# Kernel optimization log

Measured on AMD Instinct MI355X. Metric: run time of the kernel, lower is better.

## Reference

```python
import jax, jax.numpy as jnp
import numpy as np

D_MODEL = 2048
N_HEADS = 16
D_HEAD = D_MODEL // N_HEADS
FF = 4 * D_MODEL
B, L = 2, 2048


def setup_inputs() -> dict:
    key = jax.random.key(0)
    ks = jax.random.split(key, 12)
    s = 0.02
    inp = {
        "x": jax.random.normal(ks[0], (B, L, D_MODEL), jnp.float32),
        "rope_cos": jnp.cos(jnp.arange(L)[:, None] / (10000.0 ** (jnp.arange(D_HEAD) / D_HEAD))).astype(jnp.float32),
        "rope_sin": jnp.sin(jnp.arange(L)[:, None] / (10000.0 ** (jnp.arange(D_HEAD) / D_HEAD))).astype(jnp.float32),
        "mask": jnp.ones((B, L), jnp.int32),
        "w_norm1": jnp.ones((D_MODEL,), jnp.float32),
        "w_norm2": jnp.ones((D_MODEL,), jnp.float32),
        # linear weights stored as [in, out] (transposed torch layout)
        "wq": jax.random.normal(ks[1], (D_MODEL, D_MODEL), jnp.float32) * s,
        "wk": jax.random.normal(ks[2], (D_MODEL, D_MODEL), jnp.float32) * s,
        "wv": jax.random.normal(ks[3], (D_MODEL, D_MODEL), jnp.float32) * s,
        "wo": jax.random.normal(ks[4], (D_MODEL, D_MODEL), jnp.float32) * s,
        "w_ff1": jax.random.normal(ks[5], (D_MODEL, FF), jnp.float32) * s,
        "w_ff2": jax.random.normal(ks[6], (FF, D_MODEL), jnp.float32) * s,
    }
    return inp


def _rmsnorm(x, w):
    eps = jnp.finfo(x.dtype).eps
    return x * jax.lax.rsqrt(jnp.mean(x * x, axis=-1, keepdims=True) + eps) * w


def _rotate_half(x):
    x1, x2 = jnp.split(x, 2, axis=-1)
    return jnp.concatenate([-x2, x1], axis=-1)


def reference(x, rope_cos, rope_sin, mask, w_norm1, w_norm2, wq, wk, wv, wo, w_ff1, w_ff2):
    b, l, d = x.shape
    h, dh = N_HEADS, D_HEAD

    residual = x
    xn = _rmsnorm(x, w_norm1)
    # project and split heads: [B, H, L, DH]
    q = (xn @ wq).reshape(b, l, h, dh).transpose(0, 2, 1, 3)
    k = (xn @ wk).reshape(b, l, h, dh).transpose(0, 2, 1, 3)
    v = (xn @ wv).reshape(b, l, h, dh).transpose(0, 2, 1, 3)

    cos = rope_cos[None, None]  # [1,1,L,DH]
    sin = rope_sin[None, None]
    q = q * cos + _rotate_half(q) * sin
    k = k * cos + _rotate_half(k) * sin

    scores = jnp.einsum("bhqd,bhkd->bhqk", q, k) * (dh ** -0.5)
    causal = jnp.tril(jnp.ones((l, l), bool))  # allowed positions
    allowed = causal[None, None] & (mask[:, None, None, :] != 0)
    scores = jnp.where(allowed, scores, -jnp.inf)
    attn = jax.nn.softmax(scores, axis=-1)  # dropout is identity in eval

    out = jnp.einsum("bhqk,bhkd->bhqd", attn, v)
    out = out.transpose(0, 2, 1, 3).reshape(b, l, d)
    x = residual + out @ wo

    xn2 = _rmsnorm(x, w_norm2)
    ff = jax.nn.silu(xn2 @ w_ff1) @ w_ff2
    return x + ff
```

## Files before the change

kernel.cpp:

```cpp
#include <hip/hip_runtime.h>


typedef __bf16 bf16;
typedef __bf16 bf16x8 __attribute__((ext_vector_type(8)));
typedef float  f32x4  __attribute__((ext_vector_type(4)));

__device__ __forceinline__ void gload16(const void* g, void* l) {
  __builtin_amdgcn_global_load_lds((const __attribute__((address_space(1))) void*)g,
                                   (__attribute__((address_space(3))) void*)l,
                                   16, 0, 0);
}

#define CBAR asm volatile("" ::: "memory")
#define WAITV(N) asm volatile("s_waitcnt vmcnt(" #N ")" ::: "memory")
#define LGKM0 asm volatile("s_waitcnt lgkmcnt(0)" ::: "memory")
#define BARR { CBAR; __builtin_amdgcn_s_barrier(); CBAR; }

__global__ __launch_bounds__(256) void rmsnorm_to_bf16(
    const float* __restrict__ x, const float* __restrict__ w, bf16* __restrict__ out)
{
  const int D = 2048;
  const int row = blockIdx.x;
  const int tid = threadIdx.x;
  const float* xr = x + (size_t)row * D;
  float4 a = ((const float4*)xr)[tid * 2];
  float4 c = ((const float4*)xr)[tid * 2 + 1];
  float ss = a.x*a.x + a.y*a.y + a.z*a.z + a.w*a.w
           + c.x*c.x + c.y*c.y + c.z*c.z + c.w*c.w;
  #pragma unroll
  for (int m = 1; m < 64; m <<= 1) ss += __shfl_xor(ss, m, 64);
  __shared__ float red[4];
  if ((tid & 63) == 0) red[tid >> 6] = ss;
  __syncthreads();
  float tot = red[0] + red[1] + red[2] + red[3];
  float rms = rsqrtf(tot * (1.0f / D) + 1.1920929e-7f);
  const float* wr = w + tid * 8;
  float vals[8] = {a.x, a.y, a.z, a.w, c.x, c.y, c.z, c.w};
  bf16x8 o;
  #pragma unroll
  for (int j = 0; j < 8; ++j) o[j] = (bf16)(vals[j] * rms * wr[j]);
  *(bf16x8*)(out + (size_t)row * D + tid * 8) = o;
}

__global__ __launch_bounds__(256) void transpose_to_bf16(
    const float* __restrict__ in, bf16* __restrict__ out, int R, int C)
{
  __shared__ float tile[32][33];
  const int tx = threadIdx.x, ty = threadIdx.y;
  const int c0 = blockIdx.x * 32, r0 = blockIdx.y * 32;
  #pragma unroll
  for (int i = 0; i < 4; ++i)
    tile[ty + i * 8][tx] = in[(size_t)(r0 + ty + i * 8) * C + c0 + tx];
  __syncthreads();
  #pragma unroll
  for (int i = 0; i < 4; ++i)
    out[(size_t)(c0 + ty + i * 8) * R + r0 + tx] = (bf16)tile[tx][ty + i * 8];
}

__global__ __launch_bounds__(256) void v_transpose(
    const bf16* __restrict__ v, bf16* __restrict__ vt)
{
  const int L = 2048, DM = 2048;
  __shared__ bf16 tile[32][33];
  const int tx = threadIdx.x, ty = threadIdx.y;
  const int k0 = blockIdx.x * 32;
  const int d0 = blockIdx.y * 32;
  const int bh = blockIdx.z;
  const int b = bh >> 4, h = bh & 15;
  #pragma unroll
  for (int i = 0; i < 4; ++i)
    tile[ty + i * 8][tx] = v[(size_t)(b * L + k0 + ty + i * 8) * DM + h * 128 + d0 + tx];
  __syncthreads();
  #pragma unroll
  for (int i = 0; i < 4; ++i) {
    const int d = d0 + ty + i * 8;
    const int key = k0 + tx;
    const int keysw = (key & ~63) | (((((key >> 3) & 7) ^ (d & 7)) << 3)) | (key & 7);
    vt[(size_t)(bh * 128 + d) * L + keysw] = tile[tx][ty + i * 8];
  }
}

template<int EPI>
__global__ __launch_bounds__(512, 1) void gemm256(
    const bf16* __restrict__ A, const bf16* __restrict__ Bt,
    void* Cout, const float* __restrict__ resid, int M, int N, int K)
{
  __shared__ bf16 sA[2][2][128 * 64];
  __shared__ bf16 sB[2][2][128 * 64];

  const int tid = threadIdx.x, lane = tid & 63, w = tid >> 6;
  const int wm = w >> 2, wn = w & 3;
  const int lo = lane & 15, hi = lane >> 4;
  const int lo7 = lo & 7;

  const int nbn = N >> 8;
  const int nwg = gridDim.x;
  int swz = blockIdx.x;
  if ((nwg & 7) == 0) { const int cpx = nwg >> 3; swz = (swz & 7) * cpx + (swz >> 3); }
  const int bm = swz / nbn, bn = swz % nbn;

  const int r0 = tid >> 3,         s0 = (tid & 7) ^ (r0 & 7);
  const int r1 = (512 + tid) >> 3, s1 = ((512 + tid) & 7) ^ (r1 & 7);
  const bf16* Ab = A  + (size_t)(bm * 256) * K;
  const bf16* Bb = Bt + (size_t)(bn * 256) * K;
  const size_t o0 = (size_t)r0 * K + s0 * 8;
  const size_t o1 = (size_t)r1 * K + s1 * 8;
  const int dst0 = (w * 64) * 8, dst1 = (512 + w * 64) * 8;
  const size_t rhK = (size_t)128 * K;

  bf16x8 a0[2][4], a1[2][4], b0[2][2], b1[2][2];
  f32x4 acc[8][4] = {};
  const int NT = K >> 6;

  auto stageA = [&](int b, int rh, int kt) {
    const bf16* s = Ab + rh * rhK + (size_t)kt * 64;
    gload16(s + o0, &sA[b][rh][dst0]);
    gload16(s + o1, &sA[b][rh][dst1]);
  };
  auto stageB = [&](int b, int rh, int kt) {
    const bf16* s = Bb + rh * rhK + (size_t)kt * 64;
    gload16(s + o0, &sB[b][rh][dst0]);
    gload16(s + o1, &sB[b][rh][dst1]);
  };
  auto loadA = [&](bf16x8 (&d)[2][4], int b, int rh) {
    #pragma unroll
    for (int ks = 0; ks < 2; ++ks)
      #pragma unroll
      for (int m = 0; m < 4; ++m) {
        const int row = wm * 64 + m * 16 + lo;
        d[ks][m] = *(const bf16x8*)&sA[b][rh][row * 64 + (((ks * 4 + hi) ^ lo7) << 3)];
      }
  };
  auto loadB = [&](bf16x8 (&d)[2][2], int b, int rh) {
    #pragma unroll
    for (int ks = 0; ks < 2; ++ks)
      #pragma unroll
      for (int nj = 0; nj < 2; ++nj) {
        const int row = wn * 32 + nj * 16 + lo;
        d[ks][nj] = *(const bf16x8*)&sB[b][rh][row * 64 + (((ks * 4 + hi) ^ lo7) << 3)];
      }
  };
  auto mfma16 = [&](bf16x8 (&a)[2][4], bf16x8 (&bf)[2][2], int mb, int nb2) {
    __builtin_amdgcn_s_setprio(1);
    #pragma unroll
    for (int ks = 0; ks < 2; ++ks)
      #pragma unroll
      for (int m = 0; m < 4; ++m)
        #pragma unroll
        for (int nj = 0; nj < 2; ++nj)
          acc[mb + m][nb2 + nj] = __builtin_amdgcn_mfma_f32_16x16x32_bf16(
              a[ks][m], bf[ks][nj], acc[mb + m][nb2 + nj], 0, 0, 0);
    __builtin_amdgcn_s_setprio(0);
  };

  stageA(0, 0, 0); stageB(0, 0, 0); stageB(0, 1, 0); stageA(0, 1, 0);
  WAITV(0);
  BARR;
  loadA(a0, 0, 0);
  loadB(b0, 0, 0);

  for (int t = 0; t < NT; ++t) {
    const int buf = t & 1, nb = buf ^ 1;
    const bool st = (t + 1 < NT);
    loadB(b1, buf, 1);
    if (st) stageA(nb, 0, t + 1);
    mfma16(a0, b0, 0, 0);
    if (st) { WAITV(2); } else { WAITV(0); }
    BARR;
    loadA(a1, buf, 1);
    if (st) stageB(nb, 0, t + 1);
    mfma16(a0, b1, 0, 2);
    BARR;
    if (st) stageB(nb, 1, t + 1);
    mfma16(a1, b1, 4, 2);
    if (st) { WAITV(2); }
    BARR;
    mfma16(a1, b0, 4, 0);
    if (st) {
      loadA(a0, nb, 0);
      loadB(b0, nb, 0);
      stageA(nb, 1, t + 1);
      WAITV(2);
    }
    BARR;
  }

  #pragma unroll
  for (int mi = 0; mi < 8; ++mi) {
    #pragma unroll
    for (int j = 0; j < 4; ++j) {
      const size_t row = (size_t)(bm * 256 + (mi >> 2) * 128 + wm * 64 + (mi & 3) * 16 + hi * 4 + j);
      #pragma unroll
      for (int ni = 0; ni < 4; ++ni) {
        const int col = bn * 256 + (ni >> 1) * 128 + wn * 32 + (ni & 1) * 16 + lo;
        const float v = acc[mi][ni][j];
        if constexpr (EPI == 2) {
          ((bf16*)Cout)[row * (size_t)N + col] = (bf16)(v / (1.0f + __expf(-v)));
        } else {
          ((bf16*)Cout)[(size_t)(col >> 11) * 8388608 + row * 2048 + (col & 2047)] = (bf16)v;
        }
      }
    }
  }
}

__global__ __launch_bounds__(512, 1) void gemm128(
    const bf16* __restrict__ A, const bf16* __restrict__ Bt,
    float* __restrict__ Cout, const float* __restrict__ resid, int M, int N, int K)
{
  __shared__ bf16 sA[2][128 * 64];
  __shared__ bf16 sB[2][2][128 * 64];

  const int tid = threadIdx.x, lane = tid & 63, w = tid >> 6;
  const int wm = w >> 2, wn = w & 3;
  const int lo = lane & 15, hi = lane >> 4;
  const int lo7 = lo & 7;

  const int nbn = N >> 8;
  const int nwg = gridDim.x;
  int swz = blockIdx.x;
  if ((nwg & 7) == 0) { const int cpx = nwg >> 3; swz = (swz & 7) * cpx + (swz >> 3); }
  const int bm = swz / nbn, bn = swz % nbn;

  const int r0 = tid >> 3,         s0 = (tid & 7) ^ (r0 & 7);
  const int r1 = (512 + tid) >> 3, s1 = ((512 + tid) & 7) ^ (r1 & 7);
  const bf16* Ab = A  + (size_t)(bm * 128) * K;
  const bf16* Bb = Bt + (size_t)(bn * 256) * K;
  const size_t o0 = (size_t)r0 * K + s0 * 8;
  const size_t o1 = (size_t)r1 * K + s1 * 8;
  const int dst0 = (w * 64) * 8, dst1 = (512 + w * 64) * 8;
  const size_t nhK = (size_t)128 * K;

  bf16x8 afA[2][4], b0[2][2], b1[2][2];
  f32x4 acc[4][4] = {};
  const int NT = K >> 6;

  auto stageA = [&](int b, int kt) {
    const bf16* s = Ab + (size_t)kt * 64;
    gload16(s + o0, &sA[b][dst0]);
    gload16(s + o1, &sA[b][dst1]);
  };
  auto stageB = [&](int b, int nh, int kt) {
    const bf16* s = Bb + nh * nhK + (size_t)kt * 64;
    gload16(s + o0, &sB[b][nh][dst0]);
    gload16(s + o1, &sB[b][nh][dst1]);
  };
  auto loadA = [&](int b) {
    #pragma unroll
    for (int ks = 0; ks < 2; ++ks)
      #pragma unroll
      for (int m = 0; m < 4; ++m) {
        const int row = wm * 64 + m * 16 + lo;
        afA[ks][m] = *(const bf16x8*)&sA[b][row * 64 + (((ks * 4 + hi) ^ lo7) << 3)];
      }
  };
  auto loadB = [&](bf16x8 (&d)[2][2], int b, int nh) {
    #pragma unroll
    for (int ks = 0; ks < 2; ++ks)
      #pragma unroll
      for (int nj = 0; nj < 2; ++nj) {
        const int row = wn * 32 + nj * 16 + lo;
        d[ks][nj] = *(const bf16x8*)&sB[b][nh][row * 64 + (((ks * 4 + hi) ^ lo7) << 3)];
      }
  };
  auto mfma16 = [&](bf16x8 (&bf)[2][2], int nb2) {
    __builtin_amdgcn_s_setprio(1);
    #pragma unroll
    for (int ks = 0; ks < 2; ++ks)
      #pragma unroll
      for (int m = 0; m < 4; ++m)
        #pragma unroll
        for (int nj = 0; nj < 2; ++nj)
          acc[m][nb2 + nj] = __builtin_amdgcn_mfma_f32_16x16x32_bf16(
              afA[ks][m], bf[ks][nj], acc[m][nb2 + nj], 0, 0, 0);
    __builtin_amdgcn_s_setprio(0);
  };

  stageA(0, 0); stageB(0, 0, 0); stageB(0, 1, 0);
  WAITV(0);
  BARR;

  for (int t = 0; t < NT; ++t) {
    const int buf = t & 1, nb = buf ^ 1;
    const bool st = (t + 1 < NT);
    loadA(buf);
    loadB(b0, buf, 0);
    if (st) stageA(nb, t + 1);
    BARR; LGKM0;
    mfma16(b0, 0);
    if (st) { WAITV(2); } else { WAITV(0); }
    BARR;
    loadB(b1, buf, 1);
    if (st) { stageB(nb, 0, t + 1); stageB(nb, 1, t + 1); }
    BARR; LGKM0;
    mfma16(b1, 2);
    if (st) { WAITV(2); }
    BARR;
  }

  #pragma unroll
  for (int mi = 0; mi < 4; ++mi) {
    #pragma unroll
    for (int j = 0; j < 4; ++j) {
      const size_t row = (size_t)(bm * 128 + wm * 64 + mi * 16 + hi * 4 + j);
      const size_t ro = row * (size_t)N;
      #pragma unroll
      for (int ni = 0; ni < 4; ++ni) {
        const int col = bn * 256 + (ni >> 1) * 128 + wn * 32 + (ni & 1) * 16 + lo;
        Cout[ro + col] = acc[mi][ni][j] + resid[ro + col];
      }
    }
  }
}

__global__ __launch_bounds__(256) void rope_qk(
    bf16* q, const bf16* __restrict__ k, bf16* __restrict__ kswz,
    const float* __restrict__ cs, const float* __restrict__ sn)
{
  const int L = 2048, DM = 2048;
  const int idx = blockIdx.x * 256 + threadIdx.x;
  const int m = idx >> 7;
  const int rem = idx & 127;
  const int h = rem >> 3, t8 = rem & 7;
  const int pos = m & (L - 1);
  const int d0 = t8 * 8;
  const float* cb = cs + (size_t)pos * 128 + d0;
  const float* sb = sn + (size_t)pos * 128 + d0;
  float4 c1a = *(const float4*)(cb);      float4 c1b = *(const float4*)(cb + 4);
  float4 c2a = *(const float4*)(cb + 64); float4 c2b = *(const float4*)(cb + 68);
  float4 s1a = *(const float4*)(sb);      float4 s1b = *(const float4*)(sb + 4);
  float4 s2a = *(const float4*)(sb + 64); float4 s2b = *(const float4*)(sb + 68);
  float c1[8] = {c1a.x,c1a.y,c1a.z,c1a.w,c1b.x,c1b.y,c1b.z,c1b.w};
  float c2[8] = {c2a.x,c2a.y,c2a.z,c2a.w,c2b.x,c2b.y,c2b.z,c2b.w};
  float s1[8] = {s1a.x,s1a.y,s1a.z,s1a.w,s1b.x,s1b.y,s1b.z,s1b.w};
  float s2[8] = {s2a.x,s2a.y,s2a.z,s2a.w,s2b.x,s2b.y,s2b.z,s2b.w};
  const size_t base = (size_t)m * DM + h * 128 + d0;

  {
    bf16x8 x1 = *(bf16x8*)(q + base);
    bf16x8 x2 = *(bf16x8*)(q + base + 64);
    bf16x8 o1, o2;
    #pragma unroll
    for (int j = 0; j < 8; ++j) {
      const float a = (float)x1[j], b = (float)x2[j];
      o1[j] = (bf16)(a * c1[j] - b * s1[j]);
      o2[j] = (bf16)(b * c2[j] + a * s2[j]);
    }
    *(bf16x8*)(q + base) = o1;
    *(bf16x8*)(q + base + 64) = o2;
  }
  {
    bf16x8 x1 = *(const bf16x8*)(k + base);
    bf16x8 x2 = *(const bf16x8*)(k + base + 64);
    bf16x8 o1, o2;
    #pragma unroll
    for (int j = 0; j < 8; ++j) {
      const float a = (float)x1[j], b = (float)x2[j];
      o1[j] = (bf16)(a * c1[j] - b * s1[j]);
      o2[j] = (bf16)(b * c2[j] + a * s2[j]);
    }
    const int s = pos & 15;
    const int p1 = t8 ^ s;
    const int p2 = (8 + t8) ^ s;
    bf16* kr = kswz + (size_t)m * DM + h * 128;
    *(bf16x8*)(kr + p1 * 8) = o1;
    *(bf16x8*)(kr + p2 * 8) = o2;
  }
}

__global__ __launch_bounds__(256, 2) void attn_fwd(
    const bf16* __restrict__ Q, const bf16* __restrict__ Kswz,
    const bf16* __restrict__ VT, const int* __restrict__ mask,
    bf16* __restrict__ O)
{
  const int L = 2048, DM = 2048;
  __shared__ bf16 Kt[2][64 * 128];
  __shared__ bf16 Vt[2][128 * 64];
  __shared__ bf16 Plds[4][16 * 64];

  const int tid = threadIdx.x, lane = tid & 63, w = tid >> 6;
  const int lo = lane & 15, hi = lane >> 4;
  const int s7 = lo & 7;
  const int n = blockIdx.x;
  const int xcd = n & 7, slot = n >> 3;
  const int bh = xcd + 8 * (slot >> 5);
  const int tile = 31 - (slot & 31);
  const int b = bh >> 4, h = bh & 15;
  const int qrow = tile * 64 + w * 16;
  const float scale = 0.08838834764831845f;
  const float NEG_INF = -__builtin_inff();

  bf16x8 qf[4];
  {
    const bf16* qb = Q + (size_t)(b * L + qrow + lo) * DM + h * 128;
    #pragma unroll
    for (int ds = 0; ds < 4; ++ds) qf[ds] = *(const bf16x8*)(qb + ds * 32 + hi * 8);
  }

  float mrow[4] = {NEG_INF, NEG_INF, NEG_INF, NEG_INF};
  float lrow[4] = {0.f, 0.f, 0.f, 0.f};
  f32x4 oacc[8] = {};

  const bf16* vsrc[4];
  const bf16* ksrc[4];
  #pragma unroll
  for (int i = 0; i < 4; ++i) {
    const int gv = i * 256 + tid;
    vsrc[i] = VT + (size_t)(bh * 128 + (gv >> 3)) * L + (gv & 7) * 8;
    const int gk = i * 256 + tid;
    ksrc[i] = Kswz + (size_t)(b * L + (gk >> 4)) * DM + h * 128 + (gk & 15) * 8;
  }

  #pragma unroll
  for (int i = 0; i < 4; ++i) {
    gload16(ksrc[i], &Kt[0][(i * 256 + w * 64) * 8]);
    gload16(vsrc[i], &Vt[0][(i * 256 + w * 64) * 8]);
  }
  __syncthreads();

  const int nkt = tile + 1;
  for (int kt = 0; kt < nkt; ++kt) {
    const int buf = kt & 1;
    if (kt + 1 < nkt) {
      #pragma unroll
      for (int i = 0; i < 4; ++i) {
        gload16(ksrc[i] + (size_t)(kt + 1) * 64 * DM, &Kt[buf ^ 1][(i * 256 + w * 64) * 8]);
        gload16(vsrc[i] + (kt + 1) * 64,              &Vt[buf ^ 1][(i * 256 + w * 64) * 8]);
      }
    }

    int mk[4];
    #pragma unroll
    for (int kb = 0; kb < 4; ++kb) mk[kb] = mask[b * L + kt * 64 + kb * 16 + lo];

    f32x4 S[4];
    __builtin_amdgcn_s_setprio(1);
    #pragma unroll
    for (int kb = 0; kb < 4; ++kb) {
      f32x4 s = {};
      #pragma unroll
      for (int ds = 0; ds < 4; ++ds) {
        const bf16x8 kf = *(const bf16x8*)&Kt[buf][(kb * 16 + lo) * 128 + (((ds * 4 + hi) ^ lo) * 8)];
        s = __builtin_amdgcn_mfma_f32_16x16x32_bf16(qf[ds], kf, s, 0, 0, 0);
      }
      S[kb] = s;
    }
    __builtin_amdgcn_s_setprio(0);

    #pragma unroll
    for (int kb = 0; kb < 4; ++kb) {
      const int kidx = kt * 64 + kb * 16 + lo;
      #pragma unroll
      for (int j = 0; j < 4; ++j) {
        const float sv = S[kb][j] * scale;
        S[kb][j] = (mk[kb] != 0 && kidx <= qrow + hi * 4 + j) ? sv : NEG_INF;
      }
    }

    float p[4][4];
    #pragma unroll
    for (int j = 0; j < 4; ++j) {
      float tm = fmaxf(fmaxf(S[0][j], S[1][j]), fmaxf(S[2][j], S[3][j]));
      tm = fmaxf(tm, __shfl_xor(tm, 1, 64));
      tm = fmaxf(tm, __shfl_xor(tm, 2, 64));
      tm = fmaxf(tm, __shfl_xor(tm, 4, 64));
      tm = fmaxf(tm, __shfl_xor(tm, 8, 64));
      const float mn = fmaxf(mrow[j], tm);
      const float mn2 = (mn == NEG_INF) ? 0.f : mn;
      const float alpha = __expf(mrow[j] - mn2);
      float ps = 0.f;
      #pragma unroll
      for (int kb = 0; kb < 4; ++kb) { p[kb][j] = __expf(S[kb][j] - mn2); ps += p[kb][j]; }
      ps += __shfl_xor(ps, 1, 64);
      ps += __shfl_xor(ps, 2, 64);
      ps += __shfl_xor(ps, 4, 64);
      ps += __shfl_xor(ps, 8, 64);
      lrow[j] = lrow[j] * alpha + ps;
      mrow[j] = mn;
      #pragma unroll
      for (int n2 = 0; n2 < 8; ++n2) oacc[n2][j] *= alpha;
    }

    #pragma unroll
    for (int kb = 0; kb < 4; ++kb)
      #pragma unroll
      for (int j = 0; j < 4; ++j) {
        const int row = hi * 4 + j;
        Plds[w][row * 64 + ((((kb * 2 + (lo >> 3)) ^ (row & 7))) << 3) + (lo & 7)] = (bf16)p[kb][j];
      }

    __builtin_amdgcn_s_setprio(1);
    #pragma unroll
    for (int ks = 0; ks < 2; ++ks) {
      const bf16x8 pa = *(const bf16x8*)&Plds[w][lo * 64 + (((ks * 4 + hi) ^ s7) << 3)];
      #pragma unroll
      for (int n2 = 0; n2 < 8; ++n2) {
        const int r = n2 * 16 + lo;
        const bf16x8 vf = *(const bf16x8*)&Vt[buf][r * 64 + (((ks * 4 + hi) ^ s7) << 3)];
        oacc[n2] = __builtin_amdgcn_mfma_f32_16x16x32_bf16(pa, vf, oacc[n2], 0, 0, 0);
      }
    }
    __builtin_amdgcn_s_setprio(0);

    __syncthreads();
  }

  float inv[4];
  #pragma unroll
  for (int j = 0; j < 4; ++j) inv[j] = (lrow[j] > 0.f) ? 1.f / lrow[j] : 0.f;
  bf16* ob = O + (size_t)(b * L + qrow) * DM + h * 128;
  #pragma unroll
  for (int n2 = 0; n2 < 8; ++n2)
    #pragma unroll
    for (int j = 0; j < 4; ++j)
      ob[(size_t)(hi * 4 + j) * DM + n2 * 16 + lo] = (bf16)(oacc[n2][j] * inv[j]);
}

extern "C" void kernel_launch(void* const* d_in, const int* in_sizes, int n_in,
                              void* d_out, int out_size, void* d_ws, size_t ws_size,
                              hipStream_t stream)
{
  (void)in_sizes; (void)n_in; (void)out_size; (void)ws_size;
  const float* x        = (const float*)d_in[0];
  const float* rope_cos = (const float*)d_in[1];
  const float* rope_sin = (const float*)d_in[2];
  const int*   mask     = (const int*)d_in[3];
  const float* w_norm1  = (const float*)d_in[4];
  const float* w_norm2  = (const float*)d_in[5];
  const float* wq       = (const float*)d_in[6];
  const float* wk       = (const float*)d_in[7];
  const float* wv       = (const float*)d_in[8];
  const float* wo       = (const float*)d_in[9];
  const float* w_ff1    = (const float*)d_in[10];
  const float* w_ff2    = (const float*)d_in[11];
  float* out = (float*)d_out;

  const int M = 4096, D = 2048, FFD = 8192;
  char* ws = (char*)d_ws;
  const size_t WSLAB = 8388608ull;
  const size_t XNB   = 16777216ull;
  bf16* wqt  = (bf16*)(ws);
  bf16* wkt  = (bf16*)(ws + WSLAB);
  bf16* wvt  = (bf16*)(ws + 2 * WSLAB);
  bf16* wot  = (bf16*)(ws + 3 * WSLAB);
  char* pool = ws + 4 * WSLAB;
  bf16* xn   = (bf16*)(pool);
  bf16* qb   = (bf16*)(pool + XNB);
  bf16* kb   = (bf16*)(pool + 2 * XNB);
  bf16* vb   = (bf16*)(pool + 3 * XNB);
  bf16* ao   = (bf16*)(pool + 4 * XNB);
  bf16* vt   = (bf16*)(pool);
  bf16* kswz = (bf16*)(pool + 3 * XNB);
  bf16* ff1t = (bf16*)(ws);
  bf16* hmid = (bf16*)(pool);
  bf16* ff2t = (bf16*)(ws);
  bf16* xn2  = (bf16*)(pool + 4 * XNB);

  const dim3 tb(32, 8);

  rmsnorm_to_bf16<<<M, 256, 0, stream>>>(x, w_norm1, xn);
  transpose_to_bf16<<<dim3(D / 32, D / 32), tb, 0, stream>>>(wq, wqt, D, D);
  transpose_to_bf16<<<dim3(D / 32, D / 32), tb, 0, stream>>>(wk, wkt, D, D);
  transpose_to_bf16<<<dim3(D / 32, D / 32), tb, 0, stream>>>(wv, wvt, D, D);
  transpose_to_bf16<<<dim3(D / 32, D / 32), tb, 0, stream>>>(wo, wot, D, D);

  gemm256<3><<<(M / 256) * (6144 / 256), 512, 0, stream>>>(xn, wqt, qb, nullptr, M, 6144, D);

  v_transpose<<<dim3(2048 / 32, 128 / 32, 32), tb, 0, stream>>>(vb, vt);

  rope_qk<<<2048, 256, 0, stream>>>(qb, kb, kswz, rope_cos, rope_sin);

  attn_fwd<<<1024, 256, 0, stream>>>(qb, kswz, vt, mask, ao);

  gemm128<<<(M / 128) * (D / 256), 512, 0, stream>>>(ao, wot, out, x, M, D, D);

  rmsnorm_to_bf16<<<M, 256, 0, stream>>>(out, w_norm2, xn2);

  transpose_to_bf16<<<dim3(FFD / 32, D / 32), tb, 0, stream>>>(w_ff1, ff1t, D, FFD);
  gemm256<2><<<(M / 256) * (FFD / 256), 512, 0, stream>>>(xn2, ff1t, hmid, nullptr, M, FFD, D);

  transpose_to_bf16<<<dim3(D / 32, FFD / 32), tb, 0, stream>>>(w_ff2, ff2t, FFD, D);
  gemm128<<<(M / 128) * (D / 256), 512, 0, stream>>>(hmid, ff2t, out, out, M, D, FFD);
}
```

Baseline: 663.3 us.

## Deepen GEMM global-to-LDS prefetch to two tiles ahead with fewer vmcnt waits

Restructures the main loops of both bf16 GEMM kernels so the global_load_lds staging runs one extra K-tile ahead. Sub-tiles of tile t+2 are issued into the just-consumed buffer and vmcnt is waited only once per iteration with a larger outstanding count. The goal is to hide global memory latency behind more MFMA work. In exchange it adds barriers with lgkmcnt(0) waits before each MFMA group, and the buffer reuse ordering is delicate, so a mistake could create a race.

```diff
diff --git a/kernel.cpp b/kernel.cpp
--- a/kernel.cpp
+++ b/kernel.cpp
@@ -154,34 +154,32 @@
   };
 
   stageA(0, 0, 0); stageB(0, 0, 0); stageB(0, 1, 0); stageA(0, 1, 0);
-  WAITV(0);
+  stageA(1, 0, 1); stageB(1, 0, 1); stageB(1, 1, 1);
+  WAITV(6);
   BARR;
-  loadA(a0, 0, 0);
-  loadB(b0, 0, 0);
 
   for (int t = 0; t < NT; ++t) {
     const int buf = t & 1, nb = buf ^ 1;
-    const bool st = (t + 1 < NT);
+    const int u = 4 * t;
+    loadA(a0, buf, 0);
+    loadB(b0, buf, 0);
+    if (u + 7 < 4 * NT) stageA(nb, 1, t + 1);
+    BARR; LGKM0;
+    mfma16(a0, b0, 0, 0);
+    BARR;
     loadB(b1, buf, 1);
-    if (st) stageA(nb, 0, t + 1);
-    mfma16(a0, b0, 0, 0);
-    if (st) { WAITV(2); } else { WAITV(0); }
+    if (u + 8 < 4 * NT) stageA(buf, 0, t + 2);
+    BARR; LGKM0;
+    mfma16(a0, b1, 0, 2);
     BARR;
     loadA(a1, buf, 1);
-    if (st) stageB(nb, 0, t + 1);
-    mfma16(a0, b1, 0, 2);
+    if (u + 9 < 4 * NT) stageB(buf, 0, t + 2);
+    BARR; LGKM0;
+    mfma16(a1, b1, 4, 2);
     BARR;
-    if (st) stageB(nb, 1, t + 1);
-    mfma16(a1, b1, 4, 2);
-    if (st) { WAITV(2); }
-    BARR;
+    if (u + 10 < 4 * NT) stageB(buf, 1, t + 2);
     mfma16(a1, b0, 4, 0);
-    if (st) {
-      loadA(a0, nb, 0);
-      loadB(b0, nb, 0);
-      stageA(nb, 1, t + 1);
-      WAITV(2);
-    }
+    if (t < NT - 2) { WAITV(6); } else if (t == NT - 2) { WAITV(0); }
     BARR;
   }
 
@@ -277,24 +275,25 @@
   };
 
   stageA(0, 0); stageB(0, 0, 0); stageB(0, 1, 0);
-  WAITV(0);
+  stageA(1, 1); stageB(1, 0, 1);
+  WAITV(4);
   BARR;
 
   for (int t = 0; t < NT; ++t) {
     const int buf = t & 1, nb = buf ^ 1;
-    const bool st = (t + 1 < NT);
+    const int u = 3 * t;
     loadA(buf);
     loadB(b0, buf, 0);
-    if (st) stageA(nb, t + 1);
+    if (u + 5 < 3 * NT) stageB(nb, 1, t + 1);
     BARR; LGKM0;
     mfma16(b0, 0);
-    if (st) { WAITV(2); } else { WAITV(0); }
     BARR;
     loadB(b1, buf, 1);
-    if (st) { stageB(nb, 0, t + 1); stageB(nb, 1, t + 1); }
+    if (u + 6 < 3 * NT) stageA(buf, t + 2);
+    if (u + 7 < 3 * NT) stageB(buf, 0, t + 2);
     BARR; LGKM0;
     mfma16(b1, 2);
-    if (st) { WAITV(2); }
+    if (t < NT - 2) { WAITV(4); } else if (t == NT - 2) { WAITV(0); }
     BARR;
   }
 
```

Result: no change. 659.9 us (-0.5%).
